# Performance work log

Measured on AMD Instinct MI355X. Metric: run time of the kernel, lower is better.

## Reference

```python
import jax, jax.numpy as jnp
import numpy as np

B, T, C = 2, 2048, 2048
N_HEAD = 16
HEAD_DIM = C // N_HEAD


def setup_inputs() -> dict:
    key = jax.random.key(0)
    ks = jax.random.split(key, 5)
    s = 1.0 / np.sqrt(C)
    return {
        "x": jax.random.normal(ks[0], (B, T, C), dtype=jnp.float32),
        "Wq": jax.random.normal(ks[1], (C, C), dtype=jnp.float32) * s,
        "bq": jnp.zeros((C,), dtype=jnp.float32),
        "Wk": jax.random.normal(ks[2], (C, C), dtype=jnp.float32) * s,
        "bk": jnp.zeros((C,), dtype=jnp.float32),
        "Wv": jax.random.normal(ks[3], (C, C), dtype=jnp.float32) * s,
        "bv": jnp.zeros((C,), dtype=jnp.float32),
        "Wp": jax.random.normal(ks[4], (C, C), dtype=jnp.float32) * s,
        "bp": jnp.zeros((C,), dtype=jnp.float32),
    }


def reference(x, Wq, bq, Wk, bk, Wv, bv, Wp, bp):
    Bx, Tx, Cx = x.shape
    # torch nn.Linear: y = x @ W.T + b
    def lin(x, W, b):
        return jnp.einsum("btc,dc->btd", x, W) + b

    def split_heads(y):  # (B,T,C) -> (B,H,T,hd)
        return y.reshape(Bx, Tx, N_HEAD, HEAD_DIM).transpose(0, 2, 1, 3)

    q = split_heads(lin(x, Wq, bq))
    k = split_heads(lin(x, Wk, bk))
    v = split_heads(lin(x, Wv, bv))

    scale = 1.0 / np.sqrt(HEAD_DIM).astype(np.float32)
    attn = jnp.einsum("bhqd,bhkd->bhqk", q, k) * scale  # (B,H,T,T)
    causal = jnp.tril(jnp.ones((Tx, Tx), dtype=bool))
    attn = jnp.where(causal[None, None], attn, -jnp.inf)
    attn = jax.nn.softmax(attn, axis=-1)
    out = jnp.einsum("bhqk,bhkd->bhqd", attn, v)  # (B,H,T,hd)
    # Faithful to original: transpose(-2,-1) swaps T and head_dim, then
    # a contiguous view reinterprets memory as (B,T,C).
    out = out.transpose(0, 1, 3, 2).reshape(Bx, Tx, Cx)
    return lin(out, Wp, bp)
```

## Files before the change

kernel.cpp:

```cpp
#include <hip/hip_runtime.h>
#include <stdint.h>

#define DEVI __device__ __forceinline__

typedef __attribute__((ext_vector_type(8))) short short8;
typedef __attribute__((ext_vector_type(4))) float f32x4;
typedef __attribute__((ext_vector_type(4))) unsigned int u32x4;

static constexpr int Bn = 2;
static constexpr int Tn = 2048;
static constexpr int Cn = 2048;
static constexpr int NH = 16;
static constexpr int HD = 128;
static constexpr int Kdim = 2048;

DEVI unsigned short f2bf(float f) {
  union { float f; unsigned u; } v; v.f = f;
  return (unsigned short)((v.u + 0x7FFFu + ((v.u >> 16) & 1u)) >> 16);
}

DEVI void gload_lds16(const void* g, void* l) {
  __builtin_amdgcn_global_load_lds(
      (const __attribute__((address_space(1))) void*)g,
      (__attribute__((address_space(3))) void*)l, 16, 0, 0);
}

__global__ __launch_bounds__(256) void cast_bf16_kernel(
    const float* __restrict__ src, unsigned short* __restrict__ dst, int n) {
  int idx = (blockIdx.x * blockDim.x + threadIdx.x) * 4;
  const int stride = gridDim.x * blockDim.x * 4;
  for (; idx < n; idx += stride) {
    f32x4 f = *(const f32x4*)(src + idx);
    unsigned short o[4];
    o[0] = f2bf(f[0]); o[1] = f2bf(f[1]); o[2] = f2bf(f[2]); o[3] = f2bf(f[3]);
    *(unsigned long long*)(dst + idx) = *(const unsigned long long*)o;
  }
}

__global__ __launch_bounds__(256) void cast4_kernel(
    const float* __restrict__ s0, const float* __restrict__ s1,
    const float* __restrict__ s2, const float* __restrict__ s3,
    unsigned short* __restrict__ d0, unsigned short* __restrict__ d1,
    unsigned short* __restrict__ d2, unsigned short* __restrict__ d3, int n) {
  const int w = blockIdx.y;
  const float* src = (w == 0) ? s0 : (w == 1) ? s1 : (w == 2) ? s2 : s3;
  unsigned short* dst = (w == 0) ? d0 : (w == 1) ? d1 : (w == 2) ? d2 : d3;
  int idx = (blockIdx.x * blockDim.x + threadIdx.x) * 4;
  const int stride = gridDim.x * blockDim.x * 4;
  for (; idx < n; idx += stride) {
    f32x4 f = *(const f32x4*)(src + idx);
    unsigned short o[4];
    o[0] = f2bf(f[0]); o[1] = f2bf(f[1]); o[2] = f2bf(f[2]); o[3] = f2bf(f[3]);
    *(unsigned long long*)(dst + idx) = *(const unsigned long long*)o;
  }
}

#define QKV_BAR() __builtin_amdgcn_s_barrier()
#define QKV_MFMA(d, a, b) d = __builtin_amdgcn_mfma_f32_16x16x32_bf16(a, b, d, 0, 0, 0)

__global__ __launch_bounds__(512, 2) void gemm_qkv_8ph_kernel(
    const unsigned short* __restrict__ X,
    const unsigned short* __restrict__ Wq_, const unsigned short* __restrict__ Wk_,
    const unsigned short* __restrict__ Wv_,
    const float* __restrict__ bq_, const float* __restrict__ bk_, const float* __restrict__ bv_,
    unsigned short* __restrict__ Qo, unsigned short* __restrict__ Ko,
    unsigned short* __restrict__ Vo) {
  constexpr int NT = Kdim / 64;
  __shared__ unsigned short L[2][2][16384];

  const int tid = threadIdx.x;
  const int wave = tid >> 6, lane = tid & 63;
  const int wm = wave >> 2, wn = wave & 3;
  const int quad = lane >> 4, lr = lane & 15;

  const int flat = (int)blockIdx.x + 24 * (int)blockIdx.y;
  const int swz = (flat & 7) * 48 + (flat >> 3);
  const int bx = swz % 24, by = swz / 24;
  const int sel = bx >> 3;
  const int n0 = (bx & 7) * 256;
  const int m0 = by * 256;
  const unsigned short* W = (sel == 0) ? Wq_ : (sel == 1) ? Wk_ : Wv_;
  const float* bias = (sel == 0) ? bq_ : (sel == 1) ? bk_ : bv_;

  f32x4 acc[8][4];
  const f32x4 zero4 = {0.f, 0.f, 0.f, 0.f};
#pragma unroll
  for (int i = 0; i < 8; ++i)
#pragma unroll
    for (int j = 0; j < 4; ++j) acc[i][j] = zero4;

  const int srow = tid >> 3;
  const int schunk = (tid & 7) ^ (srow & 7);
  const unsigned short* Asrc = X + (size_t)(m0 + srow) * Kdim + schunk * 8;
  const unsigned short* Bsrc = W + (size_t)(n0 + srow) * Kdim + schunk * 8;

  auto STAGE_A = [&](int buf, int h, int t) {
    unsigned short* d = &L[buf][0][h * 8192 + tid * 8];
    const unsigned short* s = Asrc + (size_t)(h * 128) * Kdim + t * 64;
    gload_lds16(s, d);
    gload_lds16(s + (size_t)64 * Kdim, d + 4096);
  };
  auto STAGE_B = [&](int buf, int h, int t) {
    unsigned short* d = &L[buf][1][h * 8192 + tid * 8];
    const unsigned short* s = Bsrc + (size_t)(h * 128) * Kdim + t * 64;
    gload_lds16(s, d);
    gload_lds16(s + (size_t)64 * Kdim, d + 4096);
  };

  const int pc0 = (quad) ^ (lr & 7);
  const int pc1 = (4 + quad) ^ (lr & 7);
  const int aoff = (wm * 128 + lr) * 64;
  const int boff = (wn * 64 + lr) * 64;
#define RDA(mi, pc) (*(const short8*)&L[cur][0][aoff + (mi) * 1024 + (pc) * 8])
#define RDB(ni, pc) (*(const short8*)&L[cur][1][boff + (ni) * 1024 + (pc) * 8])

  STAGE_A(0, 0, 0); STAGE_A(0, 1, 0);
  STAGE_B(0, 0, 0); STAGE_B(0, 1, 0);
  STAGE_B(1, 0, 1); STAGE_B(1, 1, 1);
  asm volatile("s_waitcnt vmcnt(4)" ::: "memory");
  QKV_BAR();

  short8 Af[4][2], B01[2][2], B23[2][2];

  for (int t = 0; t < NT; ++t) {
    const int cur = t & 1, nxt = cur ^ 1;
#pragma unroll
    for (int m = 0; m < 4; ++m) { Af[m][0] = RDA(m, pc0); Af[m][1] = RDA(m, pc1); }
#pragma unroll
    for (int n = 0; n < 2; ++n) { B01[n][0] = RDB(n, pc0); B01[n][1] = RDB(n, pc1); }
    if (t + 1 < NT) STAGE_A(nxt, 0, t + 1);
    QKV_BAR();
    __builtin_amdgcn_s_setprio(1);
#pragma unroll
    for (int m = 0; m < 4; ++m)
#pragma unroll
      for (int n = 0; n < 2; ++n) {
        QKV_MFMA(acc[m][n], Af[m][0], B01[n][0]);
        QKV_MFMA(acc[m][n], Af[m][1], B01[n][1]);
      }
    __builtin_amdgcn_s_setprio(0);
    QKV_BAR();
#pragma unroll
    for (int n = 0; n < 2; ++n) { B23[n][0] = RDB(n + 2, pc0); B23[n][1] = RDB(n + 2, pc1); }
    if (t + 1 < NT) STAGE_A(nxt, 1, t + 1);
    QKV_BAR();
    __builtin_amdgcn_s_setprio(1);
#pragma unroll
    for (int m = 0; m < 4; ++m)
#pragma unroll
      for (int n = 0; n < 2; ++n) {
        QKV_MFMA(acc[m][n + 2], Af[m][0], B23[n][0]);
        QKV_MFMA(acc[m][n + 2], Af[m][1], B23[n][1]);
      }
    __builtin_amdgcn_s_setprio(0);
    QKV_BAR();
#pragma unroll
    for (int m = 0; m < 4; ++m) { Af[m][0] = RDA(m + 4, pc0); Af[m][1] = RDA(m + 4, pc1); }
    if (t + 2 < NT) STAGE_B(cur, 0, t + 2);
    QKV_BAR();
    __builtin_amdgcn_s_setprio(1);
#pragma unroll
    for (int m = 0; m < 4; ++m)
#pragma unroll
      for (int n = 0; n < 2; ++n) {
        QKV_MFMA(acc[m + 4][n], Af[m][0], B01[n][0]);
        QKV_MFMA(acc[m + 4][n], Af[m][1], B01[n][1]);
      }
    __builtin_amdgcn_s_setprio(0);
    QKV_BAR();
    if (t + 2 < NT) STAGE_B(cur, 1, t + 2);
    QKV_BAR();
    __builtin_amdgcn_s_setprio(1);
#pragma unroll
    for (int m = 0; m < 4; ++m)
#pragma unroll
      for (int n = 0; n < 2; ++n) {
        QKV_MFMA(acc[m + 4][n + 2], Af[m][0], B23[n][0]);
        QKV_MFMA(acc[m + 4][n + 2], Af[m][1], B23[n][1]);
      }
    __builtin_amdgcn_s_setprio(0);
    if (t < NT - 2) { asm volatile("s_waitcnt vmcnt(4)" ::: "memory"); }
    else            { asm volatile("s_waitcnt vmcnt(0)" ::: "memory"); }
    QKV_BAR();
  }
#undef RDA
#undef RDB

  if (sel == 2) {
#pragma unroll
    for (int ni = 0; ni < 4; ++ni) {
      const int n = n0 + wn * 64 + ni * 16 + lr;
      const float bv = bias[n];
      const int h = n >> 7, d = n & 127;
#pragma unroll
      for (int mi = 0; mi < 8; ++mi) {
        const int m = m0 + wm * 128 + mi * 16 + quad * 4;
        const int b = m >> 11, tt = m & 2047;
        unsigned short o4[4];
#pragma unroll
        for (int r = 0; r < 4; ++r) o4[r] = f2bf(acc[mi][ni][r] + bv);
        *(unsigned long long*)&Vo[(((size_t)(b * NH + h)) * HD + d) * Tn + tt] =
            *(const unsigned long long*)o4;
      }
    }
  } else {
    unsigned short* Out = (sel == 0) ? Qo : Ko;
#pragma unroll
    for (int ni = 0; ni < 4; ++ni) {
      const int n = n0 + wn * 64 + ni * 16 + lr;
      const float bv = bias[n];
      const int h = n >> 7, d = n & 127;
#pragma unroll
      for (int mi = 0; mi < 8; ++mi) {
#pragma unroll
        for (int r = 0; r < 4; ++r) {
          const int m = m0 + wm * 128 + mi * 16 + quad * 4 + r;
          const int b = m >> 11, tt = m & 2047;
          Out[(((size_t)(b * NH + h)) * Tn + tt) * HD + d] = f2bf(acc[mi][ni][r] + bv);
        }
      }
    }
  }
}

__global__ __launch_bounds__(256) void gemm_proj_kernel(
    const unsigned short* __restrict__ Aall,
    const unsigned short* __restrict__ W,
    const float* __restrict__ bias,
    float* __restrict__ Y) {
  __shared__ unsigned short As[128 * 32];
  __shared__ unsigned short Bs[128 * 32];
  const int tid = threadIdx.x;
  const int wave = tid >> 6, lane = tid & 63;
  const int wm = wave >> 1, wn = wave & 1;
  const int quad = lane >> 4, lr = lane & 15;

  const int m0 = blockIdx.y * 128, n0 = blockIdx.x * 128;
  const int bz = blockIdx.z;
  const unsigned short* A = Aall + (size_t)bz * Cn * Tn;

  f32x4 acc[4][4];
  const f32x4 zero4 = {0.f, 0.f, 0.f, 0.f};
#pragma unroll
  for (int i = 0; i < 4; ++i)
#pragma unroll
    for (int j = 0; j < 4; ++j) acc[i][j] = zero4;

  const int srow = tid >> 2;
  const int scol = (((tid & 3) ^ ((srow >> 1) & 3)) * 8);
  const unsigned short* Ag = A + (size_t)(m0 + srow) * Kdim + scol;
  const unsigned short* Bg = W + (size_t)(n0 + srow) * Kdim + scol;
  unsigned short* Al = &As[tid * 8];
  unsigned short* Bl = &Bs[tid * 8];
  const int fsw = (quad ^ ((lr >> 1) & 3)) * 8;

  for (int k0 = 0; k0 < Kdim; k0 += 32) {
    gload_lds16(Ag + k0, Al);
    gload_lds16(Ag + (size_t)64 * Kdim + k0, Al + 2048);
    gload_lds16(Bg + k0, Bl);
    gload_lds16(Bg + (size_t)64 * Kdim + k0, Bl + 2048);
    __syncthreads();
    short8 af[4], bf[4];
#pragma unroll
    for (int mi = 0; mi < 4; ++mi)
      af[mi] = *(const short8*)&As[(wm * 64 + mi * 16 + lr) * 32 + fsw];
#pragma unroll
    for (int ni = 0; ni < 4; ++ni)
      bf[ni] = *(const short8*)&Bs[(wn * 64 + ni * 16 + lr) * 32 + fsw];
#pragma unroll
    for (int mi = 0; mi < 4; ++mi)
#pragma unroll
      for (int ni = 0; ni < 4; ++ni)
        acc[mi][ni] = __builtin_amdgcn_mfma_f32_16x16x32_bf16(af[mi], bf[ni], acc[mi][ni], 0, 0, 0);
    __syncthreads();
  }

#pragma unroll
  for (int ni = 0; ni < 4; ++ni) {
    const int n = n0 + wn * 64 + ni * 16 + lr;
    const float bv = bias[n];
#pragma unroll
    for (int mi = 0; mi < 4; ++mi) {
#pragma unroll
      for (int r = 0; r < 4; ++r) {
        const int m = m0 + wm * 64 + mi * 16 + quad * 4 + r;
        Y[((size_t)bz * Tn + m) * Cn + n] = acc[mi][ni][r] + bv;
      }
    }
  }
}

__global__ __launch_bounds__(256, 1) void attn_kernel(
    const unsigned short* __restrict__ Q,
    const unsigned short* __restrict__ K,
    const unsigned short* __restrict__ V,
    unsigned short* __restrict__ Ot) {
  constexpr int KST = 136;
  constexpr int VST = 136;
  constexpr int PST = 136;
  __shared__ unsigned short Ks[128 * KST];
  __shared__ unsigned short Vs[144 * VST];
  __shared__ unsigned short Ps[128 * PST];

  const int tid = threadIdx.x;
  const int wave = tid >> 6, lane = tid & 63;
  const int quad = lane >> 4, lr = lane & 15;
  const int bh = blockIdx.y;
  const float SL = 0.08838834764831845f * 1.4426950408889634f;

  const unsigned short* Kp = K + (size_t)bh * Tn * HD;
  const unsigned short* Vp = V + (size_t)bh * HD * Tn;
  unsigned short* Pw = &Ps[wave * 32 * PST];

  for (int i = tid; i < 16 * VST; i += 256) Vs[128 * VST + i] = 0x3F80;

  const int r = tid >> 1;
  const int cc = (tid & 1) * 64;
  unsigned short* kl = &Ks[r * KST + cc];
  unsigned short* vl = &Vs[r * VST + cc];
  u32x4 kreg[8], vreg[8];

  const f32x4 zero4 = {0.f, 0.f, 0.f, 0.f};
#pragma unroll 1
  for (int half = 0; half < 2; ++half) {
    const int jt = half ? (15 - (int)blockIdx.x) : (int)blockIdx.x;
    const int q0 = jt * 128;

    const unsigned short* Qp = Q + ((size_t)bh * Tn + q0 + wave * 32) * HD;
    short8 qf[2][4];
#pragma unroll
    for (int mi = 0; mi < 2; ++mi)
#pragma unroll
      for (int ks = 0; ks < 4; ++ks)
        qf[mi][ks] = *(const short8*)&Qp[(mi * 16 + lr) * HD + ks * 32 + quad * 8];

    f32x4 oacc[2][9];
#pragma unroll
    for (int mi = 0; mi < 2; ++mi)
#pragma unroll
      for (int nd = 0; nd < 9; ++nd) oacc[mi][nd] = zero4;

    const int nch = q0 / 128 + 1;

    {
      const unsigned short* kg = &Kp[(size_t)r * HD + cc];
      const unsigned short* vg = &Vp[(size_t)r * Tn + cc];
#pragma unroll
      for (int p = 0; p < 8; ++p) {
        kreg[p] = *(const u32x4*)(kg + p * 8);
        vreg[p] = *(const u32x4*)(vg + p * 8);
      }
    }

    for (int c = 0; c < nch; ++c) {
      const int k0 = c * 128;
#pragma unroll
      for (int p = 0; p < 8; ++p) {
        *(u32x4*)(kl + p * 8) = kreg[p];
        *(u32x4*)(vl + p * 8) = vreg[p];
      }
      __syncthreads();
      if (c + 1 < nch) {
        const int k1 = k0 + 128;
        const unsigned short* kg = &Kp[(size_t)(k1 + r) * HD + cc];
        const unsigned short* vg = &Vp[(size_t)r * Tn + k1 + cc];
#pragma unroll
        for (int p = 0; p < 8; ++p) {
          kreg[p] = *(const u32x4*)(kg + p * 8);
          vreg[p] = *(const u32x4*)(vg + p * 8);
        }
      }

      f32x4 sa[2][8];
#pragma unroll
      for (int mi = 0; mi < 2; ++mi)
#pragma unroll
        for (int nt = 0; nt < 8; ++nt) sa[mi][nt] = zero4;
#pragma unroll
      for (int nt = 0; nt < 8; ++nt) {
        short8 kf[4];
#pragma unroll
        for (int ks = 0; ks < 4; ++ks)
          kf[ks] = *(const short8*)&Ks[(nt * 16 + lr) * KST + ks * 32 + quad * 8];
#pragma unroll
        for (int mi = 0; mi < 2; ++mi)
#pragma unroll
          for (int ks = 0; ks < 4; ++ks)
            sa[mi][nt] = __builtin_amdgcn_mfma_f32_16x16x32_bf16(qf[mi][ks], kf[ks], sa[mi][nt], 0, 0, 0);
      }

      if (k0 == q0) {
#pragma unroll
        for (int mi = 0; mi < 2; ++mi)
#pragma unroll
          for (int nt = 0; nt < 8; ++nt)
#pragma unroll
            for (int r2 = 0; r2 < 4; ++r2) {
              const int qg = q0 + wave * 32 + mi * 16 + quad * 4 + r2;
              const int kg = k0 + nt * 16 + lr;
              if (kg > qg) sa[mi][nt][r2] = -3.0e38f;
            }
      }

#pragma unroll
      for (int mi = 0; mi < 2; ++mi)
#pragma unroll
        for (int nt = 0; nt < 8; ++nt)
#pragma unroll
          for (int r2 = 0; r2 < 4; ++r2) {
            const float p = __builtin_amdgcn_exp2f(sa[mi][nt][r2] * SL);
            Pw[(mi * 16 + quad * 4 + r2) * PST + nt * 16 + lr] = f2bf(p);
          }

#pragma unroll
      for (int kt = 0; kt < 4; ++kt) {
        short8 pf[2];
#pragma unroll
        for (int mi = 0; mi < 2; ++mi)
          pf[mi] = *(const short8*)&Pw[(mi * 16 + lr) * PST + kt * 32 + quad * 8];
#pragma unroll
        for (int nd = 0; nd < 9; ++nd) {
          short8 vf = *(const short8*)&Vs[(nd * 16 + lr) * VST + kt * 32 + quad * 8];
#pragma unroll
          for (int mi = 0; mi < 2; ++mi)
            oacc[mi][nd] = __builtin_amdgcn_mfma_f32_16x16x32_bf16(pf[mi], vf, oacc[mi][nd], 0, 0, 0);
        }
      }
      __syncthreads();
    }

#pragma unroll
    for (int mi = 0; mi < 2; ++mi)
#pragma unroll
      for (int r2 = 0; r2 < 4; ++r2) {
        const float rl = 1.0f / oacc[mi][8][r2];
        const int tl = wave * 32 + mi * 16 + quad * 4 + r2;
#pragma unroll
        for (int nd = 0; nd < 8; ++nd)
          Ps[tl * PST + nd * 16 + lr] = f2bf(oacc[mi][nd][r2] * rl);
      }
    __syncthreads();
    {
      unsigned short* Od = Ot + (size_t)bh * HD * Tn + q0;
#pragma unroll
      for (int p = 0; p < 8; ++p) {
        const int d = p * 16 + (tid >> 4);
        const int t8 = (tid & 15) * 8;
        alignas(16) unsigned short v[8];
#pragma unroll
        for (int j = 0; j < 8; ++j) v[j] = Ps[(t8 + j) * PST + d];
        *(u32x4*)&Od[(size_t)d * Tn + t8] = *(const u32x4*)v;
      }
    }
    __syncthreads();
  }
}

extern "C" void kernel_launch(void* const* d_in, const int* in_sizes, int n_in,
                              void* d_out, int out_size, void* d_ws, size_t ws_size,
                              hipStream_t stream) {
  const float* x  = (const float*)d_in[0];
  const float* Wq = (const float*)d_in[1];
  const float* bq = (const float*)d_in[2];
  const float* Wk = (const float*)d_in[3];
  const float* bk = (const float*)d_in[4];
  const float* Wv = (const float*)d_in[5];
  const float* bv = (const float*)d_in[6];
  const float* Wp = (const float*)d_in[7];
  const float* bp = (const float*)d_in[8];
  float* out = (float*)d_out;

  char* ws = (char*)d_ws;
  const size_t MB = 1ull << 20;
  unsigned short* Xbf = (unsigned short*)(ws);
  unsigned short* Wqb = (unsigned short*)(ws + 16 * MB);
  unsigned short* Wkb = (unsigned short*)(ws + 24 * MB);
  unsigned short* Wvb = (unsigned short*)(ws + 32 * MB);
  unsigned short* Wpb = (unsigned short*)(ws + 40 * MB);
  unsigned short* Qb  = (unsigned short*)(ws + 48 * MB);
  unsigned short* Kb  = (unsigned short*)(ws + 64 * MB);
  unsigned short* Vtb = (unsigned short*)(ws + 80 * MB);
  unsigned short* Otb = (unsigned short*)(ws + 96 * MB);

  cast_bf16_kernel<<<dim3(1024), dim3(256), 0, stream>>>(x, Xbf, Bn * Tn * Cn);
  cast4_kernel<<<dim3(512, 4), dim3(256), 0, stream>>>(
      Wq, Wk, Wv, Wp, Wqb, Wkb, Wvb, Wpb, Cn * Cn);

  gemm_qkv_8ph_kernel<<<dim3(24, 16), dim3(512), 0, stream>>>(
      Xbf, Wqb, Wkb, Wvb, bq, bk, bv, Qb, Kb, Vtb);

  attn_kernel<<<dim3(8, Bn * NH), dim3(256), 0, stream>>>(Qb, Kb, Vtb, Otb);

  gemm_proj_kernel<<<dim3(16, 16, 2), dim3(256), 0, stream>>>(Otb, Wpb, bp, out);
}
```

Before: 416.9 us.

## Retile QKV GEMM to 256x192 over fused weights and rewrite projection GEMM

The QKV GEMM now treats Wq/Wk/Wv as one contiguous 6144-row weight, indexed through the Wqb pointer that relies on the workspace layout, and uses 256x192 tiles on a 32x16 grid of 512 blocks. This is meant to fill the CUs more evenly than the previous 384-block grid. The projection GEMM moves from a simple 128x128, 256-thread, single-buffered kernel with a barrier every K step to a 256x128, 512-thread, double-buffered, swizzled pipeline matching the QKV kernel. The fused-weight indexing depends on Wq, Wk and Wv being adjacent in the workspace, and the larger tiles raise register pressure.

```diff
diff --git a/kernel.cpp b/kernel.cpp
--- a/kernel.cpp
+++ b/kernel.cpp
@@ -55,143 +55,122 @@
   }
 }
 
-#define QKV_BAR() __builtin_amdgcn_s_barrier()
-#define QKV_MFMA(d, a, b) d = __builtin_amdgcn_mfma_f32_16x16x32_bf16(a, b, d, 0, 0, 0)
-
-__global__ __launch_bounds__(512, 2) void gemm_qkv_8ph_kernel(
+#define G_BAR() __builtin_amdgcn_s_barrier()
+#define G_MFMA(d, a, b) d = __builtin_amdgcn_mfma_f32_16x16x32_bf16(a, b, d, 0, 0, 0)
+
+__global__ __launch_bounds__(512, 2) void gemm_qkv_256x192_kernel(
     const unsigned short* __restrict__ X,
-    const unsigned short* __restrict__ Wq_, const unsigned short* __restrict__ Wk_,
-    const unsigned short* __restrict__ Wv_,
+    const unsigned short* __restrict__ W3,
     const float* __restrict__ bq_, const float* __restrict__ bk_, const float* __restrict__ bv_,
     unsigned short* __restrict__ Qo, unsigned short* __restrict__ Ko,
     unsigned short* __restrict__ Vo) {
   constexpr int NT = Kdim / 64;
-  __shared__ unsigned short L[2][2][16384];
+  __shared__ unsigned short L[2][28672];
 
   const int tid = threadIdx.x;
   const int wave = tid >> 6, lane = tid & 63;
   const int wm = wave >> 2, wn = wave & 3;
   const int quad = lane >> 4, lr = lane & 15;
 
-  const int flat = (int)blockIdx.x + 24 * (int)blockIdx.y;
-  const int swz = (flat & 7) * 48 + (flat >> 3);
-  const int bx = swz % 24, by = swz / 24;
-  const int sel = bx >> 3;
-  const int n0 = (bx & 7) * 256;
+  const int flat = (int)blockIdx.x + 32 * (int)blockIdx.y;
+  const int swz = (flat & 7) * 64 + (flat >> 3);
+  const int bx = swz & 31, by = swz >> 5;
+  const int n0 = bx * 192;
   const int m0 = by * 256;
-  const unsigned short* W = (sel == 0) ? Wq_ : (sel == 1) ? Wk_ : Wv_;
-  const float* bias = (sel == 0) ? bq_ : (sel == 1) ? bk_ : bv_;
-
-  f32x4 acc[8][4];
+
+  f32x4 acc[8][3];
   const f32x4 zero4 = {0.f, 0.f, 0.f, 0.f};
 #pragma unroll
   for (int i = 0; i < 8; ++i)
 #pragma unroll
-    for (int j = 0; j < 4; ++j) acc[i][j] = zero4;
+    for (int j = 0; j < 3; ++j) acc[i][j] = zero4;
 
   const int srow = tid >> 3;
   const int schunk = (tid & 7) ^ (srow & 7);
   const unsigned short* Asrc = X + (size_t)(m0 + srow) * Kdim + schunk * 8;
-  const unsigned short* Bsrc = W + (size_t)(n0 + srow) * Kdim + schunk * 8;
-
-  auto STAGE_A = [&](int buf, int h, int t) {
-    unsigned short* d = &L[buf][0][h * 8192 + tid * 8];
-    const unsigned short* s = Asrc + (size_t)(h * 128) * Kdim + t * 64;
-    gload_lds16(s, d);
-    gload_lds16(s + (size_t)64 * Kdim, d + 4096);
+  const unsigned short* Bsrc = W3 + (size_t)(n0 + srow) * Kdim + schunk * 8;
+
+  auto STAGE_A = [&](int buf, int t) {
+    unsigned short* d = &L[buf][tid * 8];
+    const unsigned short* s = Asrc + t * 64;
+#pragma unroll
+    for (int h = 0; h < 4; ++h)
+      gload_lds16(s + (size_t)(h * 64) * Kdim, d + h * 4096);
   };
-  auto STAGE_B = [&](int buf, int h, int t) {
-    unsigned short* d = &L[buf][1][h * 8192 + tid * 8];
-    const unsigned short* s = Bsrc + (size_t)(h * 128) * Kdim + t * 64;
-    gload_lds16(s, d);
-    gload_lds16(s + (size_t)64 * Kdim, d + 4096);
+  auto STAGE_B = [&](int buf, int t) {
+    unsigned short* d = &L[buf][16384 + tid * 8];
+    const unsigned short* s = Bsrc + t * 64;
+#pragma unroll
+    for (int h = 0; h < 3; ++h)
+      gload_lds16(s + (size_t)(h * 64) * Kdim, d + h * 4096);
   };
 
-  const int pc0 = (quad) ^ (lr & 7);
+  const int pc0 = quad ^ (lr & 7);
   const int pc1 = (4 + quad) ^ (lr & 7);
   const int aoff = (wm * 128 + lr) * 64;
-  const int boff = (wn * 64 + lr) * 64;
-#define RDA(mi, pc) (*(const short8*)&L[cur][0][aoff + (mi) * 1024 + (pc) * 8])
-#define RDB(ni, pc) (*(const short8*)&L[cur][1][boff + (ni) * 1024 + (pc) * 8])
-
-  STAGE_A(0, 0, 0); STAGE_A(0, 1, 0);
-  STAGE_B(0, 0, 0); STAGE_B(0, 1, 0);
-  STAGE_B(1, 0, 1); STAGE_B(1, 1, 1);
-  asm volatile("s_waitcnt vmcnt(4)" ::: "memory");
-  QKV_BAR();
-
-  short8 Af[4][2], B01[2][2], B23[2][2];
+  const int boff = 16384 + (wn * 48 + lr) * 64;
+
+  STAGE_A(0, 0);
+  STAGE_B(0, 0);
+  STAGE_B(1, 1);
+  asm volatile("s_waitcnt vmcnt(3)" ::: "memory");
+  G_BAR();
+
+  short8 Af[4][2], Bf[3][2];
 
   for (int t = 0; t < NT; ++t) {
     const int cur = t & 1, nxt = cur ^ 1;
 #pragma unroll
-    for (int m = 0; m < 4; ++m) { Af[m][0] = RDA(m, pc0); Af[m][1] = RDA(m, pc1); }
-#pragma unroll
-    for (int n = 0; n < 2; ++n) { B01[n][0] = RDB(n, pc0); B01[n][1] = RDB(n, pc1); }
-    if (t + 1 < NT) STAGE_A(nxt, 0, t + 1);
-    QKV_BAR();
+    for (int m = 0; m < 4; ++m) {
+      Af[m][0] = *(const short8*)&L[cur][aoff + m * 1024 + pc0 * 8];
+      Af[m][1] = *(const short8*)&L[cur][aoff + m * 1024 + pc1 * 8];
+    }
+#pragma unroll
+    for (int n = 0; n < 3; ++n) {
+      Bf[n][0] = *(const short8*)&L[cur][boff + n * 1024 + pc0 * 8];
+      Bf[n][1] = *(const short8*)&L[cur][boff + n * 1024 + pc1 * 8];
+    }
+    if (t + 1 < NT) STAGE_A(nxt, t + 1);
+    G_BAR();
     __builtin_amdgcn_s_setprio(1);
 #pragma unroll
     for (int m = 0; m < 4; ++m)
 #pragma unroll
-      for (int n = 0; n < 2; ++n) {
-        QKV_MFMA(acc[m][n], Af[m][0], B01[n][0]);
-        QKV_MFMA(acc[m][n], Af[m][1], B01[n][1]);
+      for (int n = 0; n < 3; ++n) {
+        G_MFMA(acc[m][n], Af[m][0], Bf[n][0]);
+        G_MFMA(acc[m][n], Af[m][1], Bf[n][1]);
       }
     __builtin_amdgcn_s_setprio(0);
-    QKV_BAR();
-#pragma unroll
-    for (int n = 0; n < 2; ++n) { B23[n][0] = RDB(n + 2, pc0); B23[n][1] = RDB(n + 2, pc1); }
-    if (t + 1 < NT) STAGE_A(nxt, 1, t + 1);
-    QKV_BAR();
+    G_BAR();
+#pragma unroll
+    for (int m = 0; m < 4; ++m) {
+      Af[m][0] = *(const short8*)&L[cur][aoff + (m + 4) * 1024 + pc0 * 8];
+      Af[m][1] = *(const short8*)&L[cur][aoff + (m + 4) * 1024 + pc1 * 8];
+    }
+    if (t + 2 < NT) STAGE_B(cur, t + 2);
+    G_BAR();
     __builtin_amdgcn_s_setprio(1);
 #pragma unroll
     for (int m = 0; m < 4; ++m)
 #pragma unroll
-      for (int n = 0; n < 2; ++n) {
-        QKV_MFMA(acc[m][n + 2], Af[m][0], B23[n][0]);
-        QKV_MFMA(acc[m][n + 2], Af[m][1], B23[n][1]);
+      for (int n = 0; n < 3; ++n) {
+        G_MFMA(acc[m + 4][n], Af[m][0], Bf[n][0]);
+        G_MFMA(acc[m + 4][n], Af[m][1], Bf[n][1]);
       }
     __builtin_amdgcn_s_setprio(0);
-    QKV_BAR();
-#pragma unroll
-    for (int m = 0; m < 4; ++m) { Af[m][0] = RDA(m + 4, pc0); Af[m][1] = RDA(m + 4, pc1); }
-    if (t + 2 < NT) STAGE_B(cur, 0, t + 2);
-    QKV_BAR();
-    __builtin_amdgcn_s_setprio(1);
-#pragma unroll
-    for (int m = 0; m < 4; ++m)
-#pragma unroll
-      for (int n = 0; n < 2; ++n) {
-        QKV_MFMA(acc[m + 4][n], Af[m][0], B01[n][0]);
-        QKV_MFMA(acc[m + 4][n], Af[m][1], B01[n][1]);
-      }
-    __builtin_amdgcn_s_setprio(0);
-    QKV_BAR();
-    if (t + 2 < NT) STAGE_B(cur, 1, t + 2);
-    QKV_BAR();
-    __builtin_amdgcn_s_setprio(1);
-#pragma unroll
-    for (int m = 0; m < 4; ++m)
-#pragma unroll
-      for (int n = 0; n < 2; ++n) {
-        QKV_MFMA(acc[m + 4][n + 2], Af[m][0], B23[n][0]);
-        QKV_MFMA(acc[m + 4][n + 2], Af[m][1], B23[n][1]);
-      }
-    __builtin_amdgcn_s_setprio(0);
-    if (t < NT - 2) { asm volatile("s_waitcnt vmcnt(4)" ::: "memory"); }
+    if (t < NT - 2) { asm volatile("s_waitcnt vmcnt(3)" ::: "memory"); }
     else            { asm volatile("s_waitcnt vmcnt(0)" ::: "memory"); }
-    QKV_BAR();
-  }
-#undef RDA
-#undef RDB
-
-  if (sel == 2) {
-#pragma unroll
-    for (int ni = 0; ni < 4; ++ni) {
-      const int n = n0 + wn * 64 + ni * 16 + lr;
-      const float bv = bias[n];
-      const int h = n >> 7, d = n & 127;
+    G_BAR();
+  }
+
+#pragma unroll
+  for (int ni = 0; ni < 3; ++ni) {
+    const int n = n0 + wn * 48 + ni * 16 + lr;
+    const int mat = n >> 11;
+    const int nl = n & 2047;
+    const int h = nl >> 7, d = nl & 127;
+    const float bv = (mat == 0 ? bq_ : mat == 1 ? bk_ : bv_)[nl];
+    if (mat == 2) {
 #pragma unroll
       for (int mi = 0; mi < 8; ++mi) {
         const int m = m0 + wm * 128 + mi * 16 + quad * 4;
@@ -202,14 +181,8 @@
         *(unsigned long long*)&Vo[(((size_t)(b * NH + h)) * HD + d) * Tn + tt] =
             *(const unsigned long long*)o4;
       }
-    }
-  } else {
-    unsigned short* Out = (sel == 0) ? Qo : Ko;
-#pragma unroll
-    for (int ni = 0; ni < 4; ++ni) {
-      const int n = n0 + wn * 64 + ni * 16 + lr;
-      const float bv = bias[n];
-      const int h = n >> 7, d = n & 127;
+    } else {
+      unsigned short* Out = (mat == 0) ? Qo : Ko;
 #pragma unroll
       for (int mi = 0; mi < 8; ++mi) {
 #pragma unroll
@@ -223,67 +196,119 @@
   }
 }
 
-__global__ __launch_bounds__(256) void gemm_proj_kernel(
+__global__ __launch_bounds__(512, 2) void gemm_proj_256x128_kernel(
     const unsigned short* __restrict__ Aall,
-    const unsigned short* __restrict__ W,
+    const unsigned short* __restrict__ Wp_,
     const float* __restrict__ bias,
     float* __restrict__ Y) {
-  __shared__ unsigned short As[128 * 32];
-  __shared__ unsigned short Bs[128 * 32];
+  constexpr int NT = Kdim / 64;
+  __shared__ unsigned short L[2][24576];
+
   const int tid = threadIdx.x;
   const int wave = tid >> 6, lane = tid & 63;
-  const int wm = wave >> 1, wn = wave & 1;
+  const int wm = wave >> 2, wn = wave & 3;
   const int quad = lane >> 4, lr = lane & 15;
 
-  const int m0 = blockIdx.y * 128, n0 = blockIdx.x * 128;
+  const int flat = (int)blockIdx.x + 16 * (int)blockIdx.y;
+  const int swz = (flat & 7) * 16 + (flat >> 3);
+  const int bx = swz % 16, by = swz / 16;
+  const int m0 = by * 256, n0 = bx * 128;
   const int bz = blockIdx.z;
   const unsigned short* A = Aall + (size_t)bz * Cn * Tn;
 
-  f32x4 acc[4][4];
+  f32x4 acc[8][2];
   const f32x4 zero4 = {0.f, 0.f, 0.f, 0.f};
 #pragma unroll
-  for (int i = 0; i < 4; ++i)
-#pragma unroll
-    for (int j = 0; j < 4; ++j) acc[i][j] = zero4;
-
-  const int srow = tid >> 2;
-  const int scol = (((tid & 3) ^ ((srow >> 1) & 3)) * 8);
-  const unsigned short* Ag = A + (size_t)(m0 + srow) * Kdim + scol;
-  const unsigned short* Bg = W + (size_t)(n0 + srow) * Kdim + scol;
-  unsigned short* Al = &As[tid * 8];
-  unsigned short* Bl = &Bs[tid * 8];
-  const int fsw = (quad ^ ((lr >> 1) & 3)) * 8;
-
-  for (int k0 = 0; k0 < Kdim; k0 += 32) {
-    gload_lds16(Ag + k0, Al);
-    gload_lds16(Ag + (size_t)64 * Kdim + k0, Al + 2048);
-    gload_lds16(Bg + k0, Bl);
-    gload_lds16(Bg + (size_t)64 * Kdim + k0, Bl + 2048);
-    __syncthreads();
-    short8 af[4], bf[4];
-#pragma unroll
-    for (int mi = 0; mi < 4; ++mi)
-      af[mi] = *(const short8*)&As[(wm * 64 + mi * 16 + lr) * 32 + fsw];
-#pragma unroll
-    for (int ni = 0; ni < 4; ++ni)
-      bf[ni] = *(const short8*)&Bs[(wn * 64 + ni * 16 + lr) * 32 + fsw];
-#pragma unroll
-    for (int mi = 0; mi < 4; ++mi)
-#pragma unroll
-      for (int ni = 0; ni < 4; ++ni)
-        acc[mi][ni] = __builtin_amdgcn_mfma_f32_16x16x32_bf16(af[mi], bf[ni], acc[mi][ni], 0, 0, 0);
-    __syncthreads();
-  }
-
-#pragma unroll
-  for (int ni = 0; ni < 4; ++ni) {
-    const int n = n0 + wn * 64 + ni * 16 + lr;
+  for (int i = 0; i < 8; ++i)
+#pragma unroll
+    for (int j = 0; j < 2; ++j) acc[i][j] = zero4;
+
+  const int srow = tid >> 3;
+  const int schunk = (tid & 7) ^ (srow & 7);
+  const unsigned short* Asrc = A + (size_t)(m0 + srow) * Kdim + schunk * 8;
+  const unsigned short* Bsrc = Wp_ + (size_t)(n0 + srow) * Kdim + schunk * 8;
+
+  auto STAGE_A = [&](int buf, int h, int t) {
+    unsigned short* d = &L[buf][h * 8192 + tid * 8];
+    const unsigned short* s = Asrc + (size_t)(h * 128) * Kdim + t * 64;
+    gload_lds16(s, d);
+    gload_lds16(s + (size_t)64 * Kdim, d + 4096);
+  };
+  auto STAGE_B = [&](int buf, int t) {
+    unsigned short* d = &L[buf][16384 + tid * 8];
+    const unsigned short* s = Bsrc + t * 64;
+    gload_lds16(s, d);
+    gload_lds16(s + (size_t)64 * Kdim, d + 4096);
+  };
+
+  const int pc0 = quad ^ (lr & 7);
+  const int pc1 = (4 + quad) ^ (lr & 7);
+  const int aoff = (wm * 128 + lr) * 64;
+  const int boff = 16384 + (wn * 32 + lr) * 64;
+
+  STAGE_A(0, 0, 0); STAGE_A(0, 1, 0);
+  STAGE_B(0, 0);
+  STAGE_B(1, 1);
+  asm volatile("s_waitcnt vmcnt(2)" ::: "memory");
+  G_BAR();
+
+  short8 Af[4][2], Bf[2][2];
+
+  for (int t = 0; t < NT; ++t) {
+    const int cur = t & 1, nxt = cur ^ 1;
+#pragma unroll
+    for (int m = 0; m < 4; ++m) {
+      Af[m][0] = *(const short8*)&L[cur][aoff + m * 1024 + pc0 * 8];
+      Af[m][1] = *(const short8*)&L[cur][aoff + m * 1024 + pc1 * 8];
+    }
+#pragma unroll
+    for (int n = 0; n < 2; ++n) {
+      Bf[n][0] = *(const short8*)&L[cur][boff + n * 1024 + pc0 * 8];
+      Bf[n][1] = *(const short8*)&L[cur][boff + n * 1024 + pc1 * 8];
+    }
+    if (t + 1 < NT) STAGE_A(nxt, 0, t + 1);
+    G_BAR();
+    __builtin_amdgcn_s_setprio(1);
+#pragma unroll
+    for (int m = 0; m < 4; ++m)
+#pragma unroll
+      for (int n = 0; n < 2; ++n) {
+        G_MFMA(acc[m][n], Af[m][0], Bf[n][0]);
+        G_MFMA(acc[m][n], Af[m][1], Bf[n][1]);
+      }
+    __builtin_amdgcn_s_setprio(0);
+    G_BAR();
+#pragma unroll
+    for (int m = 0; m < 4; ++m) {
+      Af[m][0] = *(const short8*)&L[cur][aoff + (m + 4) * 1024 + pc0 * 8];
+      Af[m][1] = *(const short8*)&L[cur][aoff + (m + 4) * 1024 + pc1 * 8];
+    }
+    if (t + 1 < NT) STAGE_A(nxt, 1, t + 1);
+    if (t + 2 < NT) STAGE_B(cur, t + 2);
+    G_BAR();
+    __builtin_amdgcn_s_setprio(1);
+#pragma unroll
+    for (int m = 0; m < 4; ++m)
+#pragma unroll
+      for (int n = 0; n < 2; ++n) {
+        G_MFMA(acc[m + 4][n], Af[m][0], Bf[n][0]);
+        G_MFMA(acc[m + 4][n], Af[m][1], Bf[n][1]);
+      }
+    __builtin_amdgcn_s_setprio(0);
+    if (t < NT - 2) { asm volatile("s_waitcnt vmcnt(2)" ::: "memory"); }
+    else            { asm volatile("s_waitcnt vmcnt(0)" ::: "memory"); }
+    G_BAR();
+  }
+
+#pragma unroll
+  for (int ni = 0; ni < 2; ++ni) {
+    const int n = n0 + wn * 32 + ni * 16 + lr;
     const float bv = bias[n];
 #pragma unroll
-    for (int mi = 0; mi < 4; ++mi) {
+    for (int mi = 0; mi < 8; ++mi) {
 #pragma unroll
       for (int r = 0; r < 4; ++r) {
-        const int m = m0 + wm * 64 + mi * 16 + quad * 4 + r;
+        const int m = m0 + wm * 128 + mi * 16 + quad * 4 + r;
         Y[((size_t)bz * Tn + m) * Cn + n] = acc[mi][ni][r] + bv;
       }
     }
@@ -486,10 +511,11 @@
   cast4_kernel<<<dim3(512, 4), dim3(256), 0, stream>>>(
       Wq, Wk, Wv, Wp, Wqb, Wkb, Wvb, Wpb, Cn * Cn);
 
-  gemm_qkv_8ph_kernel<<<dim3(24, 16), dim3(512), 0, stream>>>(
-      Xbf, Wqb, Wkb, Wvb, bq, bk, bv, Qb, Kb, Vtb);
+  gemm_qkv_256x192_kernel<<<dim3(32, 16), dim3(512), 0, stream>>>(
+      Xbf, Wqb , bq, bk, bv, Qb, Kb, Vtb);
 
   attn_kernel<<<dim3(8, Bn * NH), dim3(256), 0, stream>>>(Qb, Kb, Vtb, Otb);
 
-  gemm_proj_kernel<<<dim3(16, 16, 2), dim3(256), 0, stream>>>(Otb, Wpb, bp, out);
-}
+  gemm_proj_256x128_kernel<<<dim3(16, 8, 2), dim3(512), 0, stream>>>(
+      Otb, Wpb, bp, out);
+}
```

Result: faster. 395.9 us (-5.0%).
